# Performance work log

Hardware: AMD Instinct MI355X
Metric: run time of the kernel (lower is better)

Reference implementation:

```python
import jax, jax.numpy as jnp
import numpy as np

B, S, H = 32, 2048, 1024


def setup_inputs() -> dict:
    key = jax.random.key(0)
    k1, k2, k3, k4, k5, k6 = jax.random.split(key, 6)
    sc = 1.0 / np.sqrt(H)
    return {
        "dec_state": jax.random.normal(k1, (B, 1, H), dtype=jnp.float32),
        "enc_state": jax.random.normal(k2, (B, S, 2 * H), dtype=jnp.float32),
        "src_length": jax.random.randint(k3, (B,), 1, S + 1, dtype=jnp.int32),
        "W_enc": jax.random.normal(k4, (H, 2 * H), dtype=jnp.float32) * sc,
        "W_dec": jax.random.normal(k5, (H, H), dtype=jnp.float32) * sc,
        "W_energy": jax.random.normal(k6, (1, H), dtype=jnp.float32) * sc,
    }


def reference(dec_state, enc_state, src_length, W_enc, W_dec, W_energy):
    # enc: [B,S,H], dec: [B,1,H]
    enc = jnp.einsum('bse,he->bsh', enc_state, W_enc)
    dec = jnp.einsum('bod,hd->boh', dec_state, W_dec)
    # energies: [B,S] -> [B,1,S]
    energies = jnp.einsum('bsh,oh->bso', jnp.tanh(dec + enc), W_energy)[..., 0]
    mask = jnp.arange(S)[None, :] < src_length[:, None]  # [B,S]
    energies = jnp.where(mask, energies, -jnp.inf)[:, None, :]  # [B,1,S]
    alphas = jax.nn.softmax(energies, axis=-1)
    context = jnp.einsum('bos,se->boe', alphas[:, 0:1, :].squeeze(1)[:, None, :].squeeze(1)[:, None, :].squeeze(1)[:, None, :], enc_state) if False else jnp.matmul(alphas, enc_state)  # [B,1,2H]
    return context, alphas
```

## Files before the change

### kernel.cpp

```cpp
#include <hip/hip_runtime.h>
#include <hip/hip_bf16.h>
#include <stdint.h>

#define B_  32
#define S_  2048
#define H_  1024
#define K_  2048
#define M_  65536

#define BM  128
#define BN  128
#define BK  32
#define LDK 40

typedef __bf16 bf16x8 __attribute__((ext_vector_type(8)));
typedef float  f32x4  __attribute__((ext_vector_type(4)));

__device__ __forceinline__ unsigned short f2bf(float x) {
    unsigned u = __builtin_bit_cast(unsigned, x);
    u += 0x7fffu + ((u >> 16) & 1u);
    return (unsigned short)(u >> 16);
}

__device__ __forceinline__ unsigned pk_bf16(float x, float y) {
#if __has_builtin(__builtin_amdgcn_cvt_pk_bf16_f32)
    auto r = __builtin_amdgcn_cvt_pk_bf16_f32(x, y);
    static_assert(sizeof(r) == 4, "cvt_pk_bf16 size");
    return __builtin_bit_cast(unsigned, r);
#else
    return ((unsigned)f2bf(x)) | ((unsigned)f2bf(y) << 16);
#endif
}

__device__ __forceinline__ float tanh_fast(float x) {
    float e = __expf(2.0f * x);
    return 1.0f - 2.0f / (e + 1.0f);
}

__global__ __launch_bounds__(256) void cast_k(const float* __restrict__ in,
                                              unsigned short* __restrict__ o, int n4) {
    int i = blockIdx.x * 256 + threadIdx.x;
    if (i < n4) {
        float4 v = *(const float4*)(in + (long)i * 4);
        uint2 pk;
        pk.x = pk_bf16(v.x, v.y);
        pk.y = pk_bf16(v.z, v.w);
        *(uint2*)(o + (long)i * 4) = pk;
    }
}

__global__ __launch_bounds__(256) void dec_k(const float* __restrict__ ds,
                                             const float* __restrict__ Wd,
                                             float* __restrict__ decv) {
    const int b = blockIdx.y;
    const int w = threadIdx.x >> 6, lane = threadIdx.x & 63;
    const int h = blockIdx.x * 4 + w;
    const float* wr = Wd + (long)h * H_;
    const float* dr = ds + (long)b * H_;
    float acc = 0.f;
#pragma unroll
    for (int i = 0; i < 4; i++) {
        int idx = lane * 4 + i * 256;
        float4 a = *(const float4*)(wr + idx);
        float4 d = *(const float4*)(dr + idx);
        acc += a.x * d.x + a.y * d.y + a.z * d.z + a.w * d.w;
    }
    for (int m2 = 1; m2 < 64; m2 <<= 1) acc += __shfl_xor(acc, m2, 64);
    if (lane == 0) decv[(long)b * H_ + h] = acc;
}

__global__ __launch_bounds__(256) void gemm_energy(const float* __restrict__ A,
                                                   const unsigned short* __restrict__ Bw,
                                                   const float* __restrict__ decv,
                                                   const float* __restrict__ Weng,
                                                   float* __restrict__ pe) {
    __shared__ __align__(16) unsigned short Asm[BM * LDK];
    __shared__ __align__(1024) unsigned short Bsm[BN * BK];
    __shared__ float esum[2][BM];

    const int L = blockIdx.x;
    const int xcd = L & 7;
    const int slot = L >> 3;
    const int nb = slot & 7;
    const int mb = (slot >> 3) * 8 + xcd;

    const int t = threadIdx.x;
    const int lane = t & 63, w = t >> 6;
    const int wm = w >> 1, wn = w & 1;
    const int r = lane & 15, g = lane >> 4;

    f32x4 acc[4][4];
#pragma unroll
    for (int mi = 0; mi < 4; mi++)
#pragma unroll
        for (int ni = 0; ni < 4; ni++)
#pragma unroll
            for (int k = 0; k < 4; k++) acc[mi][ni][k] = 0.f;

    const float* Abase = A + (long)mb * BM * K_;
    const unsigned short* Bbase = Bw + (long)nb * BN * K_;

    for (int kt = 0; kt < K_; kt += BK) {
        __syncthreads();
#pragma unroll
        for (int j = 0; j < 2; j++) {
            int u = t + 256 * j;
            int row = u >> 2, c8 = (u & 3) << 3;
            __builtin_amdgcn_global_load_lds(
                (const __attribute__((address_space(1))) unsigned*)(Bbase + (long)row * K_ + kt + c8),
                (__attribute__((address_space(3))) unsigned*)&Bsm[u * 8],
                16, 0, 0);
        }
#pragma unroll
        for (int i = 0; i < 4; i++) {
            int f = t + 256 * i;
            int row = f >> 3, c4 = (f & 7) << 2;
            float4 v = *(const float4*)(Abase + (long)row * K_ + kt + c4);
            uint2 pk;
            pk.x = pk_bf16(v.x, v.y);
            pk.y = pk_bf16(v.z, v.w);
            *(uint2*)&Asm[row * LDK + c4] = pk;
        }
        __syncthreads();
        bf16x8 af[4], bfr[4];
#pragma unroll
        for (int mi = 0; mi < 4; mi++)
            af[mi] = *(const bf16x8*)&Asm[(wm * 64 + mi * 16 + r) * LDK + g * 8];
#pragma unroll
        for (int ni = 0; ni < 4; ni++)
            bfr[ni] = *(const bf16x8*)&Bsm[(wn * 64 + ni * 16 + r) * BK + g * 8];
#pragma unroll
        for (int mi = 0; mi < 4; mi++)
#pragma unroll
            for (int ni = 0; ni < 4; ni++)
                acc[mi][ni] = __builtin_amdgcn_mfma_f32_16x16x32_bf16(af[mi], bfr[ni],
                                                                     acc[mi][ni], 0, 0, 0);
    }

    const int b = mb >> 4;
    float wv[4], dv[4];
#pragma unroll
    for (int ni = 0; ni < 4; ni++) {
        int h = nb * BN + wn * 64 + ni * 16 + r;
        wv[ni] = Weng[h];
        dv[ni] = decv[b * H_ + h];
    }
    float rs[4][4];
#pragma unroll
    for (int mi = 0; mi < 4; mi++)
#pragma unroll
        for (int rr = 0; rr < 4; rr++) rs[mi][rr] = 0.f;
#pragma unroll
    for (int mi = 0; mi < 4; mi++)
#pragma unroll
        for (int ni = 0; ni < 4; ni++)
#pragma unroll
            for (int rr = 0; rr < 4; rr++)
                rs[mi][rr] += wv[ni] * tanh_fast(dv[ni] + acc[mi][ni][rr]);
#pragma unroll
    for (int m2 = 1; m2 < 16; m2 <<= 1)
#pragma unroll
        for (int mi = 0; mi < 4; mi++)
#pragma unroll
            for (int rr = 0; rr < 4; rr++)
                rs[mi][rr] += __shfl_xor(rs[mi][rr], m2, 64);
    if (r == 0) {
#pragma unroll
        for (int mi = 0; mi < 4; mi++)
#pragma unroll
            for (int rr = 0; rr < 4; rr++)
                esum[wn][wm * 64 + mi * 16 + g * 4 + rr] = rs[mi][rr];
    }
    __syncthreads();
    if (t < BM) pe[(long)nb * M_ + (long)mb * BM + t] = esum[0][t] + esum[1][t];
}

__global__ __launch_bounds__(256) void softmax_k(const float* __restrict__ pe,
                                                 const int* __restrict__ slen,
                                                 float* __restrict__ alph) {
    const int b = blockIdx.x, t = threadIdx.x;
    const int len = slen[b];
    __shared__ float sh[4];
    const float NEG = -__builtin_inff();
    float e[8];
    float mx = NEG;
#pragma unroll
    for (int i = 0; i < 8; i++) {
        int s = t + i * 256;
        float v = 0.f;
#pragma unroll
        for (int p = 0; p < 8; p++) v += pe[(long)p * M_ + b * S_ + s];
        v = (s < len) ? v : NEG;
        e[i] = v;
        mx = fmaxf(mx, v);
    }
    for (int m2 = 1; m2 < 64; m2 <<= 1) mx = fmaxf(mx, __shfl_xor(mx, m2, 64));
    if ((t & 63) == 0) sh[t >> 6] = mx;
    __syncthreads();
    mx = fmaxf(fmaxf(sh[0], sh[1]), fmaxf(sh[2], sh[3]));
    float sum = 0.f;
#pragma unroll
    for (int i = 0; i < 8; i++) {
        float x = (e[i] == NEG) ? 0.f : __expf(e[i] - mx);
        e[i] = x;
        sum += x;
    }
    for (int m2 = 1; m2 < 64; m2 <<= 1) sum += __shfl_xor(sum, m2, 64);
    __syncthreads();
    if ((t & 63) == 0) sh[t >> 6] = sum;
    __syncthreads();
    sum = sh[0] + sh[1] + sh[2] + sh[3];
    float inv = 1.0f / sum;
#pragma unroll
    for (int i = 0; i < 8; i++) alph[b * S_ + t + i * 256] = e[i] * inv;
}

__global__ __launch_bounds__(256) void context_k(const float* __restrict__ enc,
                                                 const float* __restrict__ alph,
                                                 const int* __restrict__ slen,
                                                 float* __restrict__ out) {
    const int b = blockIdx.y;
    const int x = blockIdx.x;
    const int ec = x & 1, sc = x >> 1;
    const int len = slen[b];
    const int s0 = sc * 256;
    if (s0 >= len) return;
    const int send = min(s0 + 256, len);
    __shared__ float al[256];
    const int t = threadIdx.x;
    al[t] = alph[b * S_ + s0 + t];
    __syncthreads();
    const int e0 = ec * 1024 + t * 4;
    float ax = 0.f, ay = 0.f, az = 0.f, aw = 0.f;
    const float* base = enc + ((long)b * S_ + s0) * K_ + e0;
#pragma unroll 4
    for (int s = s0; s < send; ++s) {
        float a = al[s - s0];
        float4 v = *(const float4*)base;
        ax += a * v.x; ay += a * v.y; az += a * v.z; aw += a * v.w;
        base += K_;
    }
    float* o = out + (long)b * K_ + e0;
    atomicAdd(o + 0, ax);
    atomicAdd(o + 1, ay);
    atomicAdd(o + 2, az);
    atomicAdd(o + 3, aw);
}

extern "C" void kernel_launch(void* const* d_in, const int* in_sizes, int n_in,
                              void* d_out, int out_size, void* d_ws, size_t ws_size,
                              hipStream_t stream) {
    const float* dec_state = (const float*)d_in[0];
    const float* enc_state = (const float*)d_in[1];
    const int*   src_len   = (const int*)d_in[2];
    const float* W_enc     = (const float*)d_in[3];
    const float* W_dec     = (const float*)d_in[4];
    const float* W_energy  = (const float*)d_in[5];
    float* out = (float*)d_out;

    char* ws = (char*)d_ws;
    float* decv = (float*)ws;
    float* pe   = (float*)(ws + 131072);
    unsigned short* Wenc_bf = (unsigned short*)(ws + 131072 + 2097152);
    float* alph = out + 65536;

    hipMemsetAsync(out, 0, 65536 * sizeof(float), stream);

    cast_k<<<2048, 256, 0, stream>>>(W_enc, Wenc_bf, 524288);
    dec_k<<<dim3(H_ / 4, B_), 256, 0, stream>>>(dec_state, W_dec, decv);
    gemm_energy<<<4096, 256, 0, stream>>>(enc_state, Wenc_bf, decv, W_energy, pe);
    softmax_k<<<B_, 256, 0, stream>>>(pe, src_len, alph);
    context_k<<<dim3(16, B_), 256, 0, stream>>>(enc_state, alph, src_len, out);
}
```

Baseline: 1.154 ms.

## Pre-cast encoder states to bf16 once and reuse in GEMM and context

Adds a pass that casts the whole fp32 encoder tensor to bf16 in workspace. A new GEMM then loads both operands straight into LDS with async global_load_lds, and the context reduction reads the bf16 copy instead of fp32. This cuts bytes read in the GEMM loop and the context pass, at the cost of one extra full read and a half-size write of the encoder tensor. It also changes the context precision to bf16 inputs. The context blocks are split finer (64 positions each) for more parallelism, and the old fp32 path is kept as a fallback when the workspace is too small.

```diff
diff --git a/kernel.cpp b/kernel.cpp
--- a/kernel.cpp
+++ b/kernel.cpp
@@ -32,20 +32,27 @@
 #endif
 }
 
+__device__ __forceinline__ float bf2f(unsigned u16) {
+    return __builtin_bit_cast(float, u16 << 16);
+}
+
 __device__ __forceinline__ float tanh_fast(float x) {
     float e = __expf(2.0f * x);
     return 1.0f - 2.0f / (e + 1.0f);
 }
 
-__global__ __launch_bounds__(256) void cast_k(const float* __restrict__ in,
-                                              unsigned short* __restrict__ o, int n4) {
-    int i = blockIdx.x * 256 + threadIdx.x;
-    if (i < n4) {
-        float4 v = *(const float4*)(in + (long)i * 4);
-        uint2 pk;
-        pk.x = pk_bf16(v.x, v.y);
-        pk.y = pk_bf16(v.z, v.w);
-        *(uint2*)(o + (long)i * 4) = pk;
+__global__ __launch_bounds__(256) void cast8_k(const float* __restrict__ in,
+                                               unsigned short* __restrict__ o, long n8) {
+    long i = (long)blockIdx.x * 256 + threadIdx.x;
+    if (i < n8) {
+        const float4* p = (const float4*)(in + i * 8);
+        float4 a = p[0], b = p[1];
+        uint4 pk;
+        pk.x = pk_bf16(a.x, a.y);
+        pk.y = pk_bf16(a.z, a.w);
+        pk.z = pk_bf16(b.x, b.y);
+        pk.w = pk_bf16(b.z, b.w);
+        *(uint4*)(o + i * 8) = pk;
     }
 }
 
@@ -69,6 +76,115 @@
     if (lane == 0) decv[(long)b * H_ + h] = acc;
 }
 
+__device__ __forceinline__ void energy_epilogue(f32x4 acc[4][4], int mb, int nb,
+                                                const float* decv, const float* Weng,
+                                                float* pe, float esum[2][BM],
+                                                int t, int wm, int wn, int r, int g) {
+    const int b = mb >> 4;
+    float wv[4], dv[4];
+#pragma unroll
+    for (int ni = 0; ni < 4; ni++) {
+        int h = nb * BN + wn * 64 + ni * 16 + r;
+        wv[ni] = Weng[h];
+        dv[ni] = decv[b * H_ + h];
+    }
+    float rs[4][4];
+#pragma unroll
+    for (int mi = 0; mi < 4; mi++)
+#pragma unroll
+        for (int rr = 0; rr < 4; rr++) rs[mi][rr] = 0.f;
+#pragma unroll
+    for (int mi = 0; mi < 4; mi++)
+#pragma unroll
+        for (int ni = 0; ni < 4; ni++)
+#pragma unroll
+            for (int rr = 0; rr < 4; rr++)
+                rs[mi][rr] += wv[ni] * tanh_fast(dv[ni] + acc[mi][ni][rr]);
+#pragma unroll
+    for (int m2 = 1; m2 < 16; m2 <<= 1)
+#pragma unroll
+        for (int mi = 0; mi < 4; mi++)
+#pragma unroll
+            for (int rr = 0; rr < 4; rr++)
+                rs[mi][rr] += __shfl_xor(rs[mi][rr], m2, 64);
+    if (r == 0) {
+#pragma unroll
+        for (int mi = 0; mi < 4; mi++)
+#pragma unroll
+            for (int rr = 0; rr < 4; rr++)
+                esum[wn][wm * 64 + mi * 16 + g * 4 + rr] = rs[mi][rr];
+    }
+    __syncthreads();
+    if (t < BM) pe[(long)nb * M_ + (long)mb * BM + t] = esum[0][t] + esum[1][t];
+}
+
+__global__ __launch_bounds__(256) void gemm_fast(const unsigned short* __restrict__ Abf,
+                                                 const unsigned short* __restrict__ Bw,
+                                                 const float* __restrict__ decv,
+                                                 const float* __restrict__ Weng,
+                                                 float* __restrict__ pe) {
+    __shared__ __align__(1024) unsigned short Asm[BM * BK];
+    __shared__ __align__(1024) unsigned short Bsm[BN * BK];
+    __shared__ float esum[2][BM];
+
+    const int L = blockIdx.x;
+    const int xcd = L & 7;
+    const int slot = L >> 3;
+    const int nb = slot & 7;
+    const int mb = (slot >> 3) * 8 + xcd;
+
+    const int t = threadIdx.x;
+    const int lane = t & 63, w = t >> 6;
+    const int wm = w >> 1, wn = w & 1;
+    const int r = lane & 15, g = lane >> 4;
+
+    f32x4 acc[4][4];
+#pragma unroll
+    for (int mi = 0; mi < 4; mi++)
+#pragma unroll
+        for (int ni = 0; ni < 4; ni++)
+#pragma unroll
+            for (int k = 0; k < 4; k++) acc[mi][ni][k] = 0.f;
+
+    const unsigned short* Abase = Abf + (long)mb * BM * K_;
+    const unsigned short* Bbase = Bw + (long)nb * BN * K_;
+
+    for (int kt = 0; kt < K_; kt += BK) {
+        __syncthreads();
+#pragma unroll
+        for (int j = 0; j < 2; j++) {
+            int u = t + 256 * j;
+            int row = u >> 2, c8 = (u & 3) << 3;
+            __builtin_amdgcn_global_load_lds(
+                (const __attribute__((address_space(1))) unsigned*)(Abase + (long)row * K_ + kt + c8),
+                (__attribute__((address_space(3))) unsigned*)&Asm[u * 8], 16, 0, 0);
+        }
+#pragma unroll
+        for (int j = 0; j < 2; j++) {
+            int u = t + 256 * j;
+            int row = u >> 2, c8 = (u & 3) << 3;
+            __builtin_amdgcn_global_load_lds(
+                (const __attribute__((address_space(1))) unsigned*)(Bbase + (long)row * K_ + kt + c8),
+                (__attribute__((address_space(3))) unsigned*)&Bsm[u * 8], 16, 0, 0);
+        }
+        __syncthreads();
+        bf16x8 af[4], bfr[4];
+#pragma unroll
+        for (int mi = 0; mi < 4; mi++)
+            af[mi] = *(const bf16x8*)&Asm[(wm * 64 + mi * 16 + r) * BK + g * 8];
+#pragma unroll
+        for (int ni = 0; ni < 4; ni++)
+            bfr[ni] = *(const bf16x8*)&Bsm[(wn * 64 + ni * 16 + r) * BK + g * 8];
+#pragma unroll
+        for (int mi = 0; mi < 4; mi++)
+#pragma unroll
+            for (int ni = 0; ni < 4; ni++)
+                acc[mi][ni] = __builtin_amdgcn_mfma_f32_16x16x32_bf16(af[mi], bfr[ni],
+                                                                     acc[mi][ni], 0, 0, 0);
+    }
+    energy_epilogue(acc, mb, nb, decv, Weng, pe, esum, t, wm, wn, r, g);
+}
+
 __global__ __launch_bounds__(256) void gemm_energy(const float* __restrict__ A,
                                                    const unsigned short* __restrict__ Bw,
                                                    const float* __restrict__ decv,
@@ -108,8 +224,7 @@
             int row = u >> 2, c8 = (u & 3) << 3;
             __builtin_amdgcn_global_load_lds(
                 (const __attribute__((address_space(1))) unsigned*)(Bbase + (long)row * K_ + kt + c8),
-                (__attribute__((address_space(3))) unsigned*)&Bsm[u * 8],
-                16, 0, 0);
+                (__attribute__((address_space(3))) unsigned*)&Bsm[u * 8], 16, 0, 0);
         }
 #pragma unroll
         for (int i = 0; i < 4; i++) {
@@ -136,43 +251,7 @@
                 acc[mi][ni] = __builtin_amdgcn_mfma_f32_16x16x32_bf16(af[mi], bfr[ni],
                                                                      acc[mi][ni], 0, 0, 0);
     }
-
-    const int b = mb >> 4;
-    float wv[4], dv[4];
-#pragma unroll
-    for (int ni = 0; ni < 4; ni++) {
-        int h = nb * BN + wn * 64 + ni * 16 + r;
-        wv[ni] = Weng[h];
-        dv[ni] = decv[b * H_ + h];
-    }
-    float rs[4][4];
-#pragma unroll
-    for (int mi = 0; mi < 4; mi++)
-#pragma unroll
-        for (int rr = 0; rr < 4; rr++) rs[mi][rr] = 0.f;
-#pragma unroll
-    for (int mi = 0; mi < 4; mi++)
-#pragma unroll
-        for (int ni = 0; ni < 4; ni++)
-#pragma unroll
-            for (int rr = 0; rr < 4; rr++)
-                rs[mi][rr] += wv[ni] * tanh_fast(dv[ni] + acc[mi][ni][rr]);
-#pragma unroll
-    for (int m2 = 1; m2 < 16; m2 <<= 1)
-#pragma unroll
-        for (int mi = 0; mi < 4; mi++)
-#pragma unroll
-            for (int rr = 0; rr < 4; rr++)
-                rs[mi][rr] += __shfl_xor(rs[mi][rr], m2, 64);
-    if (r == 0) {
-#pragma unroll
-        for (int mi = 0; mi < 4; mi++)
-#pragma unroll
-            for (int rr = 0; rr < 4; rr++)
-                esum[wn][wm * 64 + mi * 16 + g * 4 + rr] = rs[mi][rr];
-    }
-    __syncthreads();
-    if (t < BM) pe[(long)nb * M_ + (long)mb * BM + t] = esum[0][t] + esum[1][t];
+    energy_epilogue(acc, mb, nb, decv, Weng, pe, esum, t, wm, wn, r, g);
 }
 
 __global__ __launch_bounds__(256) void softmax_k(const float* __restrict__ pe,
@@ -215,24 +294,60 @@
     for (int i = 0; i < 8; i++) alph[b * S_ + t + i * 256] = e[i] * inv;
 }
 
-__global__ __launch_bounds__(256) void context_k(const float* __restrict__ enc,
-                                                 const float* __restrict__ alph,
-                                                 const int* __restrict__ slen,
-                                                 float* __restrict__ out) {
-    const int b = blockIdx.y;
-    const int x = blockIdx.x;
-    const int ec = x & 1, sc = x >> 1;
+__global__ __launch_bounds__(256) void context_bf(const unsigned short* __restrict__ encbf,
+                                                  const float* __restrict__ alph,
+                                                  const int* __restrict__ slen,
+                                                  float* __restrict__ out) {
+    const int slot = blockIdx.x;
+    const int b = slot & 31, sc = slot >> 5;
     const int len = slen[b];
-    const int s0 = sc * 256;
+    const int s0 = sc * 64;
     if (s0 >= len) return;
-    const int send = min(s0 + 256, len);
-    __shared__ float al[256];
+    const int send = min(s0 + 64, len);
+    __shared__ float al[64];
     const int t = threadIdx.x;
-    al[t] = alph[b * S_ + s0 + t];
+    if (t < 64) al[t] = alph[b * S_ + s0 + t];
+    __syncthreads();
+    const unsigned short* base = encbf + ((long)b * S_ + s0) * K_ + t * 8;
+    float ac[8];
+#pragma unroll
+    for (int j = 0; j < 8; j++) ac[j] = 0.f;
+#pragma unroll 4
+    for (int s = s0; s < send; ++s) {
+        float a = al[s - s0];
+        uint4 v = *(const uint4*)base;
+        ac[0] += a * bf2f(v.x & 0xffffu);
+        ac[1] += a * bf2f(v.x >> 16);
+        ac[2] += a * bf2f(v.y & 0xffffu);
+        ac[3] += a * bf2f(v.y >> 16);
+        ac[4] += a * bf2f(v.z & 0xffffu);
+        ac[5] += a * bf2f(v.z >> 16);
+        ac[6] += a * bf2f(v.w & 0xffffu);
+        ac[7] += a * bf2f(v.w >> 16);
+        base += K_;
+    }
+    float* o = out + (long)b * K_ + t * 8;
+#pragma unroll
+    for (int j = 0; j < 8; j++) atomicAdd(o + j, ac[j]);
+}
+
+__global__ __launch_bounds__(256) void context_f32(const float* __restrict__ enc,
+                                                   const float* __restrict__ alph,
+                                                   const int* __restrict__ slen,
+                                                   float* __restrict__ out) {
+    const int slot = blockIdx.x;
+    const int b = slot & 31, ec = (slot >> 5) & 1, sc = slot >> 6;
+    const int len = slen[b];
+    const int s0 = sc * 64;
+    if (s0 >= len) return;
+    const int send = min(s0 + 64, len);
+    __shared__ float al[64];
+    const int t = threadIdx.x;
+    if (t < 64) al[t] = alph[b * S_ + s0 + t];
     __syncthreads();
     const int e0 = ec * 1024 + t * 4;
+    const float* base = enc + ((long)b * S_ + s0) * K_ + e0;
     float ax = 0.f, ay = 0.f, az = 0.f, aw = 0.f;
-    const float* base = enc + ((long)b * S_ + s0) * K_ + e0;
 #pragma unroll 4
     for (int s = s0; s < send; ++s) {
         float a = al[s - s0];
@@ -260,15 +375,26 @@
 
     char* ws = (char*)d_ws;
     float* decv = (float*)ws;
-    float* pe   = (float*)(ws + 131072);
-    unsigned short* Wenc_bf = (unsigned short*)(ws + 131072 + 2097152);
+    float* pe   = (float*)(ws + (1 << 17));
+    unsigned short* Wenc_bf = (unsigned short*)(ws + 3 * (1 << 20));
+    unsigned short* Abf = (unsigned short*)(ws + 8 * (1 << 20));
     float* alph = out + 65536;
 
+    const size_t need_fast = 8ull * (1 << 20) + (size_t)M_ * K_ * 2;
+
     hipMemsetAsync(out, 0, 65536 * sizeof(float), stream);
 
-    cast_k<<<2048, 256, 0, stream>>>(W_enc, Wenc_bf, 524288);
+    cast8_k<<<1024, 256, 0, stream>>>(W_enc, Wenc_bf, (long)H_ * K_ / 8);
     dec_k<<<dim3(H_ / 4, B_), 256, 0, stream>>>(dec_state, W_dec, decv);
-    gemm_energy<<<4096, 256, 0, stream>>>(enc_state, Wenc_bf, decv, W_energy, pe);
-    softmax_k<<<B_, 256, 0, stream>>>(pe, src_len, alph);
-    context_k<<<dim3(16, B_), 256, 0, stream>>>(enc_state, alph, src_len, out);
-}
+
+    if (ws_size >= need_fast) {
+        cast8_k<<<65536, 256, 0, stream>>>(enc_state, Abf, (long)M_ * K_ / 8);
+        gemm_fast<<<4096, 256, 0, stream>>>(Abf, Wenc_bf, decv, W_energy, pe);
+        softmax_k<<<B_, 256, 0, stream>>>(pe, src_len, alph);
+        context_bf<<<1024, 256, 0, stream>>>(Abf, alph, src_len, out);
+    } else {
+        gemm_energy<<<4096, 256, 0, stream>>>(enc_state, Wenc_bf, decv, W_energy, pe);
+        softmax_k<<<B_, 256, 0, stream>>>(pe, src_len, alph);
+        context_f32<<<2048, 256, 0, stream>>>(enc_state, alph, src_len, out);
+    }
+}
```

Measured after the change: 1.130 ms. 2.1% less time.
